# Performance work log

Hardware: AMD Instinct MI355X
Metric: run time of the kernel (lower is better)

Reference implementation:

```python
import jax, jax.numpy as jnp
import numpy as np

BATCH, N_AGENTS, OBS_DIM, ACTOR_DIM, N_ACTIONS = 8192, 64, 128, 64, 32


def setup_inputs() -> dict:
    key = jax.random.key(0)
    ks = jax.random.split(key, 14)
    s = 0.05
    inp = {
        "O": jax.random.normal(ks[0], (BATCH, N_AGENTS, OBS_DIM), dtype=jnp.float32),
        "W_enc": jax.random.normal(ks[1], (OBS_DIM, ACTOR_DIM), dtype=jnp.float32) * s,
        "b_enc": jax.random.normal(ks[2], (ACTOR_DIM,), dtype=jnp.float32) * s,
        "W1": jax.random.normal(ks[3], (2 * ACTOR_DIM, ACTOR_DIM), dtype=jnp.float32) * s,
        "b1": jax.random.normal(ks[4], (ACTOR_DIM,), dtype=jnp.float32) * s,
        "W2": jax.random.normal(ks[5], (2 * ACTOR_DIM, ACTOR_DIM), dtype=jnp.float32) * s,
        "b2": jax.random.normal(ks[6], (ACTOR_DIM,), dtype=jnp.float32) * s,
        "W3": jax.random.normal(ks[7], (2 * ACTOR_DIM, ACTOR_DIM), dtype=jnp.float32) * s,
        "b3": jax.random.normal(ks[8], (ACTOR_DIM,), dtype=jnp.float32) * s,
        "W4": jax.random.normal(ks[9], (2 * ACTOR_DIM, ACTOR_DIM), dtype=jnp.float32) * s,
        "b4": jax.random.normal(ks[10], (ACTOR_DIM,), dtype=jnp.float32) * s,
        "W_dec": jax.random.normal(ks[11], (N_AGENTS * ACTOR_DIM, N_ACTIONS), dtype=jnp.float32) * s,
        "b_dec": jax.random.normal(ks[12], (N_ACTIONS,), dtype=jnp.float32) * s,
    }
    return inp


def _comm_layer(H, W, b, n_agents):
    # get_commvar: masked mean over other agents, but divided by n_agents
    # (the zeroed self term is included in the mean denominator) ->
    # C_i = (sum_j H_j - H_i) / n_agents, exactly equal to the original math.
    C = (jnp.sum(H, axis=1, keepdims=True) - H) / n_agents  # [B, A, D]
    Hcat = jnp.concatenate([H, C], axis=-1)                 # [B, A, 2D]
    return Hcat @ W + b                                     # no activation (faithful)


def reference(O, W_enc, b_enc, W1, b1, W2, b2, W3, b3, W4, b4, W_dec, b_dec):
    B, A, _ = O.shape
    H = jax.nn.sigmoid(O @ W_enc + b_enc)  # [B, A, D]
    H = _comm_layer(H, W1, b1, A)
    H = _comm_layer(H, W2, b2, A)
    H = _comm_layer(H, W3, b3, A)
    H = _comm_layer(H, W4, b4, A)
    Hf = H.reshape(B, -1)                  # [B, A*D]
    return Hf @ W_dec + b_dec              # [B, n_actions]
```

## Files before the change

### kernel.cpp

```cpp
#include <hip/hip_runtime.h>
#include <hip/hip_bf16.h>
#include <stdint.h>


#define BATCHN 8192

typedef __attribute__((ext_vector_type(8))) short short8;
typedef __attribute__((ext_vector_type(4))) float floatx4;

__device__ __forceinline__ unsigned short f2b(float f) {
    union { float f; uint32_t u; } v; v.f = f;
    uint32_t r = v.u + 0x7FFFu + ((v.u >> 16) & 1u);
    return (unsigned short)(r >> 16);
}

__device__ __forceinline__ uint32_t pk2(float x, float y) {
    float2 t; t.x = x; t.y = y;
    __hip_bfloat162 h = __float22bfloat162_rn(t);
    union { __hip_bfloat162 h; uint32_t u; } c; c.h = h;
    return c.u;
}

#define OFF_WENC 0
#define OFF_WCAT 16384
#define OFF_WDEC 81920
#define OFF_H4   344064

__global__ __launch_bounds__(256) void prep_kernel(
    const float* __restrict__ Wenc,
    const float* __restrict__ W1, const float* __restrict__ W2,
    const float* __restrict__ W3, const float* __restrict__ W4,
    const float* __restrict__ Wdec,
    unsigned short* __restrict__ ws)
{
    int tid = blockIdx.x * 256 + threadIdx.x;
    if (tid < 8192) {
        int n = tid >> 7, k = tid & 127;
        ws[OFF_WENC/2 + n*128 + k] = f2b(Wenc[k*64 + n]);
    } else if (tid < 5*8192) {
        int l = (tid - 8192) >> 13;
        int e = (tid - 8192) & 8191;
        int n = e >> 7, k = e & 127;
        const float* W = (l==0) ? W1 : (l==1) ? W2 : (l==2) ? W3 : W4;
        float v = W[k*64 + n];
        if (k < 64) v -= W[(k+64)*64 + n] * (1.0f/64.0f);
        ws[OFF_WCAT/2 + l*8192 + n*128 + k] = f2b(v);
    } else {
        int e = tid - 5*8192;
        int n = e >> 12, k = e & 4095;
        ws[OFF_WDEC/2 + n*4096 + k] = f2b(Wdec[k*32 + n]);
    }
}

__global__ __launch_bounds__(256, 2) void fused2_kernel(
    const float* __restrict__ O,
    const unsigned short* __restrict__ WencT,
    const unsigned short* __restrict__ WcatT,
    const float* __restrict__ b_enc,
    const float* __restrict__ b1, const float* __restrict__ b2,
    const float* __restrict__ b3, const float* __restrict__ b4,
    unsigned short* __restrict__ H4out)
{
    __shared__ unsigned short sH[4][64*72];
    __shared__ unsigned short sS[4][72];

    const int t = threadIdx.x, lane = t & 63, w = t >> 6;
    const int m = lane & 15, q = lane >> 4;
    const int b = blockIdx.x * 4 + w;
    unsigned short* myH = sH[w];
    unsigned short* myS = sS[w];

    float bias[5][4];
    {
        const float* bp[5] = {b_enc, b1, b2, b3, b4};
        #pragma unroll
        for (int l = 0; l < 5; l++)
            #pragma unroll
            for (int nt = 0; nt < 4; nt++)
                bias[l][nt] = bp[l][nt*16 + m];
    }

    floatx4 acc[4][4];
    short8  Bf[16];

    #pragma unroll
    for (int nt = 0; nt < 4; nt++)
        #pragma unroll
        for (int s = 0; s < 4; s++)
            Bf[nt*4+s] = *(const short8*)(WencT + (nt*16+m)*128 + s*32 + q*8);

    #pragma unroll
    for (int mt = 0; mt < 4; mt++)
        #pragma unroll
        for (int nt = 0; nt < 4; nt++)
            acc[mt][nt] = (floatx4){bias[0][nt], bias[0][nt], bias[0][nt], bias[0][nt]};

    const float* Ob = O + (size_t)b * 8192;
    #pragma unroll
    for (int s = 0; s < 4; s++) {
        short8 A[4];
        #pragma unroll
        for (int mt = 0; mt < 4; mt++) {
            const float* pr = Ob + (mt*16+m)*128 + s*32 + q*8;
            float4 f0 = *(const float4*)pr;
            float4 f1 = *(const float4*)(pr + 4);
            uint32_t* pa = (uint32_t*)&A[mt];
            pa[0] = pk2(f0.x, f0.y); pa[1] = pk2(f0.z, f0.w);
            pa[2] = pk2(f1.x, f1.y); pa[3] = pk2(f1.z, f1.w);
        }
        #pragma unroll
        for (int mt = 0; mt < 4; mt++)
            #pragma unroll
            for (int nt = 0; nt < 4; nt++)
                acc[mt][nt] = __builtin_amdgcn_mfma_f32_16x16x32_bf16(A[mt], Bf[nt*4+s], acc[mt][nt], 0, 0, 0);
    }
    #pragma unroll
    for (int mt = 0; mt < 4; mt++)
        #pragma unroll
        for (int nt = 0; nt < 4; nt++)
            #pragma unroll
            for (int r = 0; r < 4; r++)
                acc[mt][nt][r] = 1.0f / (1.0f + __expf(-acc[mt][nt][r]));

    #pragma unroll
    for (int l = 1; l <= 4; l++) {
        #pragma unroll
        for (int nt = 0; nt < 4; nt++) {
            float s = 0.f;
            #pragma unroll
            for (int mt = 0; mt < 4; mt++)
                #pragma unroll
                for (int r = 0; r < 4; r++) s += acc[mt][nt][r];
            s += __shfl_xor(s, 16, 64);
            s += __shfl_xor(s, 32, 64);
            if (q == 0) myS[nt*16 + m] = f2b(s * (1.0f/64.0f));
        }
        #pragma unroll
        for (int mt = 0; mt < 4; mt++)
            #pragma unroll
            for (int nt = 0; nt < 4; nt++) {
                uint32_t p01 = pk2(acc[mt][nt][0], acc[mt][nt][1]);
                uint32_t p23 = pk2(acc[mt][nt][2], acc[mt][nt][3]);
                unsigned short* base = myH + (mt*16 + q*4)*72 + nt*16 + m;
                base[0]   = (unsigned short)p01;
                base[72]  = (unsigned short)(p01 >> 16);
                base[144] = (unsigned short)p23;
                base[216] = (unsigned short)(p23 >> 16);
            }

        #pragma unroll
        for (int nt = 0; nt < 4; nt++)
            #pragma unroll
            for (int s = 0; s < 4; s++)
                Bf[nt*4+s] = *(const short8*)(WcatT + (l-1)*8192 + (nt*16+m)*128 + s*32 + q*8);

        #pragma unroll
        for (int mt = 0; mt < 4; mt++)
            #pragma unroll
            for (int nt = 0; nt < 4; nt++)
                acc[mt][nt] = (floatx4){bias[l][nt], bias[l][nt], bias[l][nt], bias[l][nt]};

        #pragma unroll
        for (int s2 = 0; s2 < 2; s2++) {
            short8 A[4];
            #pragma unroll
            for (int mt = 0; mt < 4; mt++)
                A[mt] = *(const short8*)(myH + (mt*16+m)*72 + s2*32 + q*8);
            #pragma unroll
            for (int mt = 0; mt < 4; mt++)
                #pragma unroll
                for (int nt = 0; nt < 4; nt++)
                    acc[mt][nt] = __builtin_amdgcn_mfma_f32_16x16x32_bf16(A[mt], Bf[nt*4+s2], acc[mt][nt], 0, 0, 0);
        }
        #pragma unroll
        for (int s2 = 0; s2 < 2; s2++) {
            short8 As = *(const short8*)(myS + s2*32 + q*8);
            #pragma unroll
            for (int mt = 0; mt < 4; mt++)
                #pragma unroll
                for (int nt = 0; nt < 4; nt++)
                    acc[mt][nt] = __builtin_amdgcn_mfma_f32_16x16x32_bf16(As, Bf[nt*4+2+s2], acc[mt][nt], 0, 0, 0);
        }
    }

    unsigned short* Hb = H4out + (size_t)b * 4096;
    #pragma unroll
    for (int mt = 0; mt < 4; mt++)
        #pragma unroll
        for (int nt = 0; nt < 4; nt++) {
            uint32_t p01 = pk2(acc[mt][nt][0], acc[mt][nt][1]);
            uint32_t p23 = pk2(acc[mt][nt][2], acc[mt][nt][3]);
            unsigned short* base = Hb + (mt*16 + q*4)*64 + nt*16 + m;
            base[0]   = (unsigned short)p01;
            base[64]  = (unsigned short)(p01 >> 16);
            base[128] = (unsigned short)p23;
            base[192] = (unsigned short)(p23 >> 16);
        }
}

__global__ __launch_bounds__(256) void dec_kernel(
    const unsigned short* __restrict__ Hf,
    const unsigned short* __restrict__ WdecT,
    const float* __restrict__ b_dec,
    float* __restrict__ out)
{
    int gt = blockIdx.x * 256 + threadIdx.x;
    int wave = gt >> 6;
    int lane = gt & 63;
    int rb = wave >> 3;
    int kc = wave & 7;
    int m = lane & 15, q = lane >> 4;

    const unsigned short* aP  = Hf    + (size_t)(rb*16 + m)*4096 + kc*512 + q*8;
    const unsigned short* bP0 = WdecT + (size_t)m*4096        + kc*512 + q*8;
    const unsigned short* bP1 = WdecT + (size_t)(16 + m)*4096 + kc*512 + q*8;

    floatx4 a0 = {0.f, 0.f, 0.f, 0.f}, a1 = {0.f, 0.f, 0.f, 0.f};
    #pragma unroll 4
    for (int s = 0; s < 16; s++) {
        short8 av  = *(const short8*)(aP  + s*32);
        short8 b0v = *(const short8*)(bP0 + s*32);
        short8 b1v = *(const short8*)(bP1 + s*32);
        a0 = __builtin_amdgcn_mfma_f32_16x16x32_bf16(av, b0v, a0, 0, 0, 0);
        a1 = __builtin_amdgcn_mfma_f32_16x16x32_bf16(av, b1v, a1, 0, 0, 0);
    }
    float bias0 = (kc == 0) ? b_dec[m]      : 0.0f;
    float bias1 = (kc == 0) ? b_dec[16 + m] : 0.0f;
    #pragma unroll
    for (int r = 0; r < 4; r++) {
        int row = rb*16 + q*4 + r;
        atomicAdd(&out[row*32 + m],      a0[r] + bias0);
        atomicAdd(&out[row*32 + 16 + m], a1[r] + bias1);
    }
}

extern "C" void kernel_launch(void* const* d_in, const int* in_sizes, int n_in,
                              void* d_out, int out_size, void* d_ws, size_t ws_size,
                              hipStream_t stream)
{
    const float* O    = (const float*)d_in[0];
    const float* Wenc = (const float*)d_in[1];
    const float* benc = (const float*)d_in[2];
    const float* W1   = (const float*)d_in[3];
    const float* b1   = (const float*)d_in[4];
    const float* W2   = (const float*)d_in[5];
    const float* b2   = (const float*)d_in[6];
    const float* W3   = (const float*)d_in[7];
    const float* b3   = (const float*)d_in[8];
    const float* W4   = (const float*)d_in[9];
    const float* b4   = (const float*)d_in[10];
    const float* Wdec = (const float*)d_in[11];
    const float* bdec = (const float*)d_in[12];
    float* out = (float*)d_out;
    unsigned short* ws = (unsigned short*)d_ws;

    hipMemsetAsync(d_out, 0, (size_t)out_size * sizeof(float), stream);
    prep_kernel<<<672, 256, 0, stream>>>(Wenc, W1, W2, W3, W4, Wdec, ws);
    fused2_kernel<<<2048, 256, 0, stream>>>(O, ws + OFF_WENC/2, ws + OFF_WCAT/2,
                                            benc, b1, b2, b3, b4, ws + OFF_H4/2);
    dec_kernel<<<1024, 256, 0, stream>>>(ws + OFF_H4/2, ws + OFF_WDEC/2, bdec, out);
}
```

Before: 474.1 us.

## Transpose MFMA roles, propagate agent-sum analytically, stream weights per k-step

Swaps the MFMA operands so weights are the A operand and agent tiles the B operand. This lets accumulator rows hold features, so the per-feature agent sum becomes an in-row shuffle and LDS/global stores become packed 8-byte writes. The agent-mean for the next layer now comes from a small extra MFMA against a precomputed summed-weight matrix (W_top + 63/64·W_bottom) instead of a reduction over the new activations. Weight fragments are loaded per k-step rather than kept in 16 registers, and launch bounds rise to 3 blocks per SM for occupancy. In exchange it adds a prep pass and a small rounding difference, since the mean is carried in bf16.

```diff
diff --git a/kernel.cpp b/kernel.cpp
--- a/kernel.cpp
+++ b/kernel.cpp
@@ -21,10 +21,11 @@
     return c.u;
 }
 
-#define OFF_WENC 0
-#define OFF_WCAT 16384
-#define OFF_WDEC 81920
-#define OFF_H4   344064
+#define U16_WENC 0
+#define U16_WCAT 8192
+#define U16_WSUM 40960
+#define U16_WDEC 57344
+#define U16_H4   188416
 
 __global__ __launch_bounds__(256) void prep_kernel(
     const float* __restrict__ Wenc,
@@ -34,168 +35,212 @@
     unsigned short* __restrict__ ws)
 {
     int tid = blockIdx.x * 256 + threadIdx.x;
+    const float* WL[4] = {W1, W2, W3, W4};
     if (tid < 8192) {
         int n = tid >> 7, k = tid & 127;
-        ws[OFF_WENC/2 + n*128 + k] = f2b(Wenc[k*64 + n]);
-    } else if (tid < 5*8192) {
-        int l = (tid - 8192) >> 13;
-        int e = (tid - 8192) & 8191;
-        int n = e >> 7, k = e & 127;
-        const float* W = (l==0) ? W1 : (l==1) ? W2 : (l==2) ? W3 : W4;
+        ws[U16_WENC + n*128 + k] = f2b(Wenc[k*64 + n]);
+    } else if (tid < 40960) {
+        int e = tid - 8192;
+        int l = e >> 13, r = e & 8191;
+        int n = r >> 7, k = r & 127;
+        const float* W = WL[l];
         float v = W[k*64 + n];
         if (k < 64) v -= W[(k+64)*64 + n] * (1.0f/64.0f);
-        ws[OFF_WCAT/2 + l*8192 + n*128 + k] = f2b(v);
+        ws[U16_WCAT + l*8192 + n*128 + k] = f2b(v);
+    } else if (tid < 57344) {
+        int e = tid - 40960;
+        int l = e >> 12, r = e & 4095;
+        int f = r >> 6, k = r & 63;
+        const float* W = WL[l];
+        float v = W[k*64 + f] + W[(k+64)*64 + f] * (63.0f/64.0f);
+        ws[U16_WSUM + l*4096 + f*64 + k] = f2b(v);
     } else {
-        int e = tid - 5*8192;
+        int e = tid - 57344;
         int n = e >> 12, k = e & 4095;
-        ws[OFF_WDEC/2 + n*4096 + k] = f2b(Wdec[k*32 + n]);
-    }
-}
-
-__global__ __launch_bounds__(256, 2) void fused2_kernel(
+        ws[U16_WDEC + n*4096 + k] = f2b(Wdec[k*32 + n]);
+    }
+}
+
+__global__ __launch_bounds__(256, 3) void fused3_kernel(
     const float* __restrict__ O,
     const unsigned short* __restrict__ WencT,
     const unsigned short* __restrict__ WcatT,
+    const unsigned short* __restrict__ WsumT,
     const float* __restrict__ b_enc,
     const float* __restrict__ b1, const float* __restrict__ b2,
     const float* __restrict__ b3, const float* __restrict__ b4,
     unsigned short* __restrict__ H4out)
 {
-    __shared__ unsigned short sH[4][64*72];
-    __shared__ unsigned short sS[4][72];
+    __shared__ unsigned short sG[4][64*72];
+    __shared__ unsigned short sS[4][64];
 
     const int t = threadIdx.x, lane = t & 63, w = t >> 6;
     const int m = lane & 15, q = lane >> 4;
     const int b = blockIdx.x * 4 + w;
-    unsigned short* myH = sH[w];
+    unsigned short* myG = sG[w];
     unsigned short* myS = sS[w];
 
-    float bias[5][4];
-    {
-        const float* bp[5] = {b_enc, b1, b2, b3, b4};
-        #pragma unroll
-        for (int l = 0; l < 5; l++)
-            #pragma unroll
-            for (int nt = 0; nt < 4; nt++)
-                bias[l][nt] = bp[l][nt*16 + m];
-    }
-
     floatx4 acc[4][4];
-    short8  Bf[16];
-
-    #pragma unroll
-    for (int nt = 0; nt < 4; nt++)
-        #pragma unroll
-        for (int s = 0; s < 4; s++)
-            Bf[nt*4+s] = *(const short8*)(WencT + (nt*16+m)*128 + s*32 + q*8);
-
-    #pragma unroll
-    for (int mt = 0; mt < 4; mt++)
-        #pragma unroll
-        for (int nt = 0; nt < 4; nt++)
-            acc[mt][nt] = (floatx4){bias[0][nt], bias[0][nt], bias[0][nt], bias[0][nt]};
+    floatx4 bb[4];
+
+    #pragma unroll
+    for (int ft = 0; ft < 4; ft++) {
+        float4 bv = *(const float4*)(b_enc + ft*16 + q*4);
+        bb[ft] = (floatx4){bv.x, bv.y, bv.z, bv.w};
+    }
+    #pragma unroll
+    for (int ft = 0; ft < 4; ft++)
+        #pragma unroll
+        for (int at = 0; at < 4; at++)
+            acc[ft][at] = bb[ft];
 
     const float* Ob = O + (size_t)b * 8192;
     #pragma unroll
     for (int s = 0; s < 4; s++) {
-        short8 A[4];
-        #pragma unroll
-        for (int mt = 0; mt < 4; mt++) {
-            const float* pr = Ob + (mt*16+m)*128 + s*32 + q*8;
+        short8 Wf[4], Bf[4];
+        #pragma unroll
+        for (int ft = 0; ft < 4; ft++)
+            Wf[ft] = *(const short8*)(WencT + (ft*16+m)*128 + s*32 + q*8);
+        #pragma unroll
+        for (int at = 0; at < 4; at++) {
+            const float* pr = Ob + (at*16+m)*128 + s*32 + q*8;
             float4 f0 = *(const float4*)pr;
             float4 f1 = *(const float4*)(pr + 4);
-            uint32_t* pa = (uint32_t*)&A[mt];
+            uint32_t* pa = (uint32_t*)&Bf[at];
             pa[0] = pk2(f0.x, f0.y); pa[1] = pk2(f0.z, f0.w);
             pa[2] = pk2(f1.x, f1.y); pa[3] = pk2(f1.z, f1.w);
         }
         #pragma unroll
-        for (int mt = 0; mt < 4; mt++)
-            #pragma unroll
-            for (int nt = 0; nt < 4; nt++)
-                acc[mt][nt] = __builtin_amdgcn_mfma_f32_16x16x32_bf16(A[mt], Bf[nt*4+s], acc[mt][nt], 0, 0, 0);
-    }
-    #pragma unroll
-    for (int mt = 0; mt < 4; mt++)
-        #pragma unroll
-        for (int nt = 0; nt < 4; nt++)
+        for (int ft = 0; ft < 4; ft++)
+            #pragma unroll
+            for (int at = 0; at < 4; at++)
+                acc[ft][at] = __builtin_amdgcn_mfma_f32_16x16x32_bf16(Wf[ft], Bf[at], acc[ft][at], 0, 0, 0);
+    }
+    #pragma unroll
+    for (int ft = 0; ft < 4; ft++)
+        #pragma unroll
+        for (int at = 0; at < 4; at++)
             #pragma unroll
             for (int r = 0; r < 4; r++)
-                acc[mt][nt][r] = 1.0f / (1.0f + __expf(-acc[mt][nt][r]));
-
-    #pragma unroll
-    for (int l = 1; l <= 4; l++) {
-        #pragma unroll
-        for (int nt = 0; nt < 4; nt++) {
-            float s = 0.f;
-            #pragma unroll
-            for (int mt = 0; mt < 4; mt++)
-                #pragma unroll
-                for (int r = 0; r < 4; r++) s += acc[mt][nt][r];
-            s += __shfl_xor(s, 16, 64);
-            s += __shfl_xor(s, 32, 64);
-            if (q == 0) myS[nt*16 + m] = f2b(s * (1.0f/64.0f));
-        }
-        #pragma unroll
-        for (int mt = 0; mt < 4; mt++)
-            #pragma unroll
-            for (int nt = 0; nt < 4; nt++) {
-                uint32_t p01 = pk2(acc[mt][nt][0], acc[mt][nt][1]);
-                uint32_t p23 = pk2(acc[mt][nt][2], acc[mt][nt][3]);
-                unsigned short* base = myH + (mt*16 + q*4)*72 + nt*16 + m;
-                base[0]   = (unsigned short)p01;
-                base[72]  = (unsigned short)(p01 >> 16);
-                base[144] = (unsigned short)p23;
-                base[216] = (unsigned short)(p23 >> 16);
+                acc[ft][at][r] = 1.0f / (1.0f + __expf(-acc[ft][at][r]));
+
+    #pragma unroll
+    for (int ft = 0; ft < 4; ft++) {
+        float tr[4];
+        #pragma unroll
+        for (int r = 0; r < 4; r++)
+            tr[r] = acc[ft][0][r] + acc[ft][1][r] + acc[ft][2][r] + acc[ft][3][r];
+        #pragma unroll
+        for (int msk = 1; msk <= 8; msk <<= 1)
+            #pragma unroll
+            for (int r = 0; r < 4; r++)
+                tr[r] += __shfl_xor(tr[r], msk, 64);
+        uint2 d;
+        d.x = pk2(tr[0] * (1.0f/64.0f), tr[1] * (1.0f/64.0f));
+        d.y = pk2(tr[2] * (1.0f/64.0f), tr[3] * (1.0f/64.0f));
+        if (m == 0) *(uint2*)&myS[ft*16 + q*4] = d;
+    }
+    #pragma unroll
+    for (int ft = 0; ft < 4; ft++)
+        #pragma unroll
+        for (int at = 0; at < 4; at++) {
+            uint2 d;
+            d.x = pk2(acc[ft][at][0], acc[ft][at][1]);
+            d.y = pk2(acc[ft][at][2], acc[ft][at][3]);
+            *(uint2*)&myG[(at*16+m)*72 + ft*16 + q*4] = d;
+        }
+
+    const float* bs_[4] = {b1, b2, b3, b4};
+    #pragma unroll
+    for (int l = 0; l < 4; l++) {
+        const unsigned short* Wl  = WcatT + l*8192;
+        const unsigned short* Wsl = WsumT + l*4096;
+        const float* bp = bs_[l];
+        #pragma unroll
+        for (int ft = 0; ft < 4; ft++) {
+            float4 bv = *(const float4*)(bp + ft*16 + q*4);
+            bb[ft] = (floatx4){bv.x, bv.y, bv.z, bv.w};
+        }
+        short8 Sf[2];
+        #pragma unroll
+        for (int s2 = 0; s2 < 2; s2++)
+            Sf[s2] = *(const short8*)&myS[s2*32 + q*8];
+
+        #pragma unroll
+        for (int ft = 0; ft < 4; ft++)
+            #pragma unroll
+            for (int at = 0; at < 4; at++)
+                acc[ft][at] = bb[ft];
+
+        #pragma unroll
+        for (int s2 = 0; s2 < 2; s2++) {
+            short8 Wf[4], Gf[4];
+            #pragma unroll
+            for (int ft = 0; ft < 4; ft++)
+                Wf[ft] = *(const short8*)(Wl + (ft*16+m)*128 + s2*32 + q*8);
+            #pragma unroll
+            for (int at = 0; at < 4; at++)
+                Gf[at] = *(const short8*)&myG[(at*16+m)*72 + s2*32 + q*8];
+            #pragma unroll
+            for (int ft = 0; ft < 4; ft++)
+                #pragma unroll
+                for (int at = 0; at < 4; at++)
+                    acc[ft][at] = __builtin_amdgcn_mfma_f32_16x16x32_bf16(Wf[ft], Gf[at], acc[ft][at], 0, 0, 0);
+        }
+        #pragma unroll
+        for (int s2 = 0; s2 < 2; s2++) {
+            short8 Wf[4];
+            #pragma unroll
+            for (int ft = 0; ft < 4; ft++)
+                Wf[ft] = *(const short8*)(Wl + (ft*16+m)*128 + (2+s2)*32 + q*8);
+            #pragma unroll
+            for (int ft = 0; ft < 4; ft++)
+                #pragma unroll
+                for (int at = 0; at < 4; at++)
+                    acc[ft][at] = __builtin_amdgcn_mfma_f32_16x16x32_bf16(Wf[ft], Sf[s2], acc[ft][at], 0, 0, 0);
+        }
+
+        if (l < 3) {
+            floatx4 sacc[4];
+            #pragma unroll
+            for (int ft = 0; ft < 4; ft++) sacc[ft] = (floatx4){0.f, 0.f, 0.f, 0.f};
+            #pragma unroll
+            for (int s2 = 0; s2 < 2; s2++) {
+                #pragma unroll
+                for (int ft = 0; ft < 4; ft++) {
+                    short8 Wsf = *(const short8*)(Wsl + (ft*16+m)*64 + s2*32 + q*8);
+                    sacc[ft] = __builtin_amdgcn_mfma_f32_16x16x32_bf16(Wsf, Sf[s2], sacc[ft], 0, 0, 0);
+                }
             }
-
-        #pragma unroll
-        for (int nt = 0; nt < 4; nt++)
-            #pragma unroll
-            for (int s = 0; s < 4; s++)
-                Bf[nt*4+s] = *(const short8*)(WcatT + (l-1)*8192 + (nt*16+m)*128 + s*32 + q*8);
-
-        #pragma unroll
-        for (int mt = 0; mt < 4; mt++)
-            #pragma unroll
-            for (int nt = 0; nt < 4; nt++)
-                acc[mt][nt] = (floatx4){bias[l][nt], bias[l][nt], bias[l][nt], bias[l][nt]};
-
-        #pragma unroll
-        for (int s2 = 0; s2 < 2; s2++) {
-            short8 A[4];
-            #pragma unroll
-            for (int mt = 0; mt < 4; mt++)
-                A[mt] = *(const short8*)(myH + (mt*16+m)*72 + s2*32 + q*8);
-            #pragma unroll
-            for (int mt = 0; mt < 4; mt++)
-                #pragma unroll
-                for (int nt = 0; nt < 4; nt++)
-                    acc[mt][nt] = __builtin_amdgcn_mfma_f32_16x16x32_bf16(A[mt], Bf[nt*4+s2], acc[mt][nt], 0, 0, 0);
-        }
-        #pragma unroll
-        for (int s2 = 0; s2 < 2; s2++) {
-            short8 As = *(const short8*)(myS + s2*32 + q*8);
-            #pragma unroll
-            for (int mt = 0; mt < 4; mt++)
-                #pragma unroll
-                for (int nt = 0; nt < 4; nt++)
-                    acc[mt][nt] = __builtin_amdgcn_mfma_f32_16x16x32_bf16(As, Bf[nt*4+2+s2], acc[mt][nt], 0, 0, 0);
-        }
-    }
-
-    unsigned short* Hb = H4out + (size_t)b * 4096;
-    #pragma unroll
-    for (int mt = 0; mt < 4; mt++)
-        #pragma unroll
-        for (int nt = 0; nt < 4; nt++) {
-            uint32_t p01 = pk2(acc[mt][nt][0], acc[mt][nt][1]);
-            uint32_t p23 = pk2(acc[mt][nt][2], acc[mt][nt][3]);
-            unsigned short* base = Hb + (mt*16 + q*4)*64 + nt*16 + m;
-            base[0]   = (unsigned short)p01;
-            base[64]  = (unsigned short)(p01 >> 16);
-            base[128] = (unsigned short)p23;
-            base[192] = (unsigned short)(p23 >> 16);
-        }
+            #pragma unroll
+            for (int ft = 0; ft < 4; ft++) {
+                uint2 d;
+                d.x = pk2(sacc[ft][0] + bb[ft][0], sacc[ft][1] + bb[ft][1]);
+                d.y = pk2(sacc[ft][2] + bb[ft][2], sacc[ft][3] + bb[ft][3]);
+                if (m == 0) *(uint2*)&myS[ft*16 + q*4] = d;
+            }
+            #pragma unroll
+            for (int ft = 0; ft < 4; ft++)
+                #pragma unroll
+                for (int at = 0; at < 4; at++) {
+                    uint2 d;
+                    d.x = pk2(acc[ft][at][0], acc[ft][at][1]);
+                    d.y = pk2(acc[ft][at][2], acc[ft][at][3]);
+                    *(uint2*)&myG[(at*16+m)*72 + ft*16 + q*4] = d;
+                }
+        } else {
+            unsigned short* Hb = H4out + (size_t)b * 4096;
+            #pragma unroll
+            for (int ft = 0; ft < 4; ft++)
+                #pragma unroll
+                for (int at = 0; at < 4; at++) {
+                    uint2 d;
+                    d.x = pk2(acc[ft][at][0], acc[ft][at][1]);
+                    d.y = pk2(acc[ft][at][2], acc[ft][at][3]);
+                    *(uint2*)(Hb + (at*16+m)*64 + ft*16 + q*4) = d;
+                }
+        }
+    }
 }
 
 __global__ __launch_bounds__(256) void dec_kernel(
@@ -255,8 +300,9 @@
     unsigned short* ws = (unsigned short*)d_ws;
 
     hipMemsetAsync(d_out, 0, (size_t)out_size * sizeof(float), stream);
-    prep_kernel<<<672, 256, 0, stream>>>(Wenc, W1, W2, W3, W4, Wdec, ws);
-    fused2_kernel<<<2048, 256, 0, stream>>>(O, ws + OFF_WENC/2, ws + OFF_WCAT/2,
-                                            benc, b1, b2, b3, b4, ws + OFF_H4/2);
-    dec_kernel<<<1024, 256, 0, stream>>>(ws + OFF_H4/2, ws + OFF_WDEC/2, bdec, out);
-}
+    prep_kernel<<<736, 256, 0, stream>>>(Wenc, W1, W2, W3, W4, Wdec, ws);
+    fused3_kernel<<<2048, 256, 0, stream>>>(O, ws + U16_WENC, ws + U16_WCAT,
+                                            ws + U16_WSUM,
+                                            benc, b1, b2, b3, b4, ws + U16_H4);
+    dec_kernel<<<1024, 256, 0, stream>>>(ws + U16_H4, ws + U16_WDEC, bdec, out);
+}
```

New measurement: 502.0 us. +5.9%, slower.
